# Kernel tuning notes

Hardware: AMD Instinct MI355X
Metric: run time of the kernel (lower is better)

Reference implementation:

```python
import jax, jax.numpy as jnp
import numpy as np

B, T, D_Q, D_V, ATTN, FILTERS, KSIZE = 64, 2048, 1024, 512, 128, 32, 31


def setup_inputs() -> dict:
    key = jax.random.key(0)
    ks = jax.random.split(key, 10)
    query = jax.random.normal(ks[0], (B, D_Q), dtype=jnp.float32)
    values = jax.random.normal(ks[1], (B, T, D_V), dtype=jnp.float32)
    keys = jax.random.normal(ks[2], (B, T, ATTN), dtype=jnp.float32)
    state = jax.random.uniform(ks[3], (B, T), dtype=jnp.float32)
    # learned parameters
    W_q = jax.random.normal(ks[4], (D_Q, ATTN), dtype=jnp.float32) * 0.02
    conv_kernel = jax.random.normal(ks[5], (KSIZE, 1, FILTERS), dtype=jnp.float32) * 0.1  # (W, In, Out)
    conv_bias = jnp.zeros((FILTERS,), dtype=jnp.float32)
    W_loc = jax.random.normal(ks[6], (FILTERS, ATTN), dtype=jnp.float32) * 0.1
    v_att = jax.random.normal(ks[7], (ATTN, 1), dtype=jnp.float32) * 0.1
    att_bias = jax.random.normal(ks[8], (ATTN,), dtype=jnp.float32) * 0.02
    return {"query": query, "values": values, "keys": keys, "state": state,
            "W_q": W_q, "conv_kernel": conv_kernel, "conv_bias": conv_bias,
            "W_loc": W_loc, "v_att": v_att, "att_bias": att_bias}


def reference(query, values, keys, state, W_q, conv_kernel, conv_bias, W_loc, v_att, att_bias):
    # processed_query: [B, 1, ATTN]
    pq = (query @ W_q)[:, None, :]
    # location features: Conv1D same-padding over alignments [B, T, 1] -> [B, T, FILTERS]
    loc = jax.lax.conv_general_dilated(
        state[:, :, None], conv_kernel,
        window_strides=(1,), padding='SAME',
        dimension_numbers=('NWC', 'WIO', 'NWC')) + conv_bias
    ploc = loc @ W_loc                                  # [B, T, ATTN]
    score = jnp.tanh(keys + pq + ploc + att_bias) @ v_att  # [B, T, 1]
    alignment = jax.nn.softmax(score, axis=1)           # [B, T, 1]
    attention = jnp.sum(alignment * values, axis=1)     # [B, D_V]
    alignment = jnp.squeeze(alignment, axis=2)          # [B, T]
    attention_state = alignment + state                 # cumulate=True
    return (attention, alignment, attention_state)
```

## Files before the change

### kernel.cpp

```cpp
#include <hip/hip_runtime.h>
#include <hip/hip_bf16.h>

#define B 64
#define T 2048
#define D_Q 1024
#define D_V 512
#define ATTN 128
#define FILTERS 32
#define KSIZE 31

#define PQ_OFF 0
#define CW_OFF 8192
#define PB_OFF (8192 + 3968)
#define SC_OFF (8192 + 3968 + 128)
#define ML_OFF (SC_OFF + 131072)
#define PART_OFF (ML_OFF + 4096)

#define AT_OFF 0
#define AL_OFF 32768
#define ST_OFF (32768 + 131072)

typedef float v4f __attribute__((ext_vector_type(4)));

__device__ __forceinline__ float4 nt_load4(const float4* p) {
    v4f v = __builtin_nontemporal_load((const v4f*)p);
    return make_float4(v.x, v.y, v.z, v.w);
}

__device__ __forceinline__ float tanh_fast(float x) {
    float e = __expf(2.f * x);
    return 1.f - 2.f / (e + 1.f);
}

__global__ void __launch_bounds__(256)
k1_precompute(const float* __restrict__ query,
              const float* __restrict__ Wq,
              const float* __restrict__ ck,
              const float* __restrict__ cbias,
              const float* __restrict__ Wl,
              const float* __restrict__ abias,
              float* __restrict__ ws) {
    int tid = threadIdx.x;
    if (blockIdx.x < B) {
        int b = blockIdx.x;
        int q = tid & 31;
        int s = tid >> 5;
        __shared__ __align__(16) float sq[D_Q];
        __shared__ float4 red[256];
        ((float4*)sq)[tid] = ((const float4*)(query + (size_t)b * D_Q))[tid];
        __syncthreads();

        const float4* Wq4 = (const float4*)Wq;
        float4 acc = make_float4(0.f, 0.f, 0.f, 0.f);
        int dbase = s << 7;
#pragma unroll 16
        for (int i = 0; i < 128; ++i) {
            int d = dbase + i;
            float sd = sq[d];
            float4 w = Wq4[(size_t)d * 32 + q];
            acc.x += sd * w.x; acc.y += sd * w.y;
            acc.z += sd * w.z; acc.w += sd * w.w;
        }
        red[tid] = acc;
        __syncthreads();
        if (tid < 128) {
            float4 o = red[tid + 128];
            acc = red[tid];
            acc.x += o.x; acc.y += o.y; acc.z += o.z; acc.w += o.w;
            red[tid] = acc;
        }
        __syncthreads();
        if (tid < 64) {
            float4 o = red[tid + 64];
            acc = red[tid];
            acc.x += o.x; acc.y += o.y; acc.z += o.z; acc.w += o.w;
            red[tid] = acc;
        }
        __syncthreads();
        if (tid < 32) {
            float4 o = red[tid + 32];
            acc = red[tid];
            acc.x += o.x; acc.y += o.y; acc.z += o.z; acc.w += o.w;
            ((float4*)(ws + PQ_OFF))[b * 32 + tid] = acc;
        }
    } else {
        __shared__ float swl[FILTERS * ATTN];
        for (int i = tid; i < FILTERS * ATTN; i += 256) swl[i] = Wl[i];
        __syncthreads();
        if (tid < ATTN) {
            int a = tid;
            for (int k = 0; k < KSIZE; ++k) {
                float acc = 0.f;
#pragma unroll
                for (int f = 0; f < FILTERS; ++f) acc += ck[k * FILTERS + f] * swl[f * ATTN + a];
                ws[CW_OFF + k * ATTN + a] = acc;
            }
            float pb = abias[a];
#pragma unroll
            for (int f = 0; f < FILTERS; ++f) pb += cbias[f] * swl[f * ATTN + a];
            ws[PB_OFF + a] = pb;
        }
    }
}

__global__ void __launch_bounds__(256)
k2_fused(const float* __restrict__ keys,
         const float* __restrict__ state,
         const float* __restrict__ values,
         const float* __restrict__ vatt,
         float* __restrict__ ws) {
    int bid = blockIdx.x;
    int b = bid >> 5;
    int c = bid & 31;
    int t0 = c << 6;
    int tid = threadIdx.x;
    int a4 = tid & 31;
    int h = tid >> 5;

    __shared__ __align__(16) float sstate[96];
    __shared__ __align__(16) float scw[KSIZE][ATTN];
    __shared__ float sred[64];
    __shared__ float sal[64];
    __shared__ float4 spart[128];

    if (tid < 96) {
        int idx = t0 + tid - 15;
        sstate[tid] = (idx >= 0 && idx < T) ? state[b * T + idx] : 0.f;
    }
    {
        const float4* cw4 = (const float4*)(ws + CW_OFF);
        float4* dst = (float4*)&scw[0][0];
        for (int i = tid; i < (KSIZE * ATTN) / 4; i += 256) dst[i] = cw4[i];
    }

    float4 pq4, vat4;
    {
        float4 pq = ((const float4*)(ws + PQ_OFF))[b * 32 + a4];
        float4 pb = ((const float4*)(ws + PB_OFF))[a4];
        pq4 = make_float4(pq.x + pb.x, pq.y + pb.y, pq.z + pb.z, pq.w + pb.w);
        vat4 = ((const float4*)vatt)[a4];
    }
    __syncthreads();

    {
        const float4* sv = (const float4*)sstate;
        float w[40];
        int wq0 = h << 1;
#pragma unroll
        for (int q = 0; q < 10; ++q) {
            float4 v = sv[wq0 + q];
            w[4 * q + 0] = v.x; w[4 * q + 1] = v.y;
            w[4 * q + 2] = v.z; w[4 * q + 3] = v.w;
        }

        const float4* K4 = (const float4*)keys
                           + ((size_t)b * T + t0 + h * 8) * (ATTN / 4) + a4;
        float4 kv[8];
#pragma unroll
        for (int j = 0; j < 8; ++j)
            kv[j] = nt_load4(&K4[(size_t)j * (ATTN / 4)]);

        float4 acc[8];
#pragma unroll
        for (int j = 0; j < 8; ++j) acc[j] = make_float4(0.f, 0.f, 0.f, 0.f);
#pragma unroll
        for (int k = 0; k < KSIZE; ++k) {
            float4 cwk = ((const float4*)&scw[k][0])[a4];
#pragma unroll
            for (int j = 0; j < 8; ++j) {
                float wv = w[j + k];
                acc[j].x += wv * cwk.x; acc[j].y += wv * cwk.y;
                acc[j].z += wv * cwk.z; acc[j].w += wv * cwk.w;
            }
        }
#pragma unroll
        for (int j = 0; j < 8; ++j) {
            float xx = kv[j].x + pq4.x + acc[j].x;
            float xy = kv[j].y + pq4.y + acc[j].y;
            float xz = kv[j].z + pq4.z + acc[j].z;
            float xw = kv[j].w + pq4.w + acc[j].w;
            float cc = tanh_fast(xx) * vat4.x + tanh_fast(xy) * vat4.y
                     + tanh_fast(xz) * vat4.z + tanh_fast(xw) * vat4.w;
#pragma unroll
            for (int off = 16; off >= 1; off >>= 1) cc += __shfl_xor(cc, off);
            if (a4 == 0) sred[h * 8 + j] = cc;
        }
    }
    __syncthreads();

    if (tid < 64) {
        float s = sred[tid];
        ws[SC_OFF + b * T + t0 + tid] = s;
        float m = s;
#pragma unroll
        for (int off = 32; off >= 1; off >>= 1) m = fmaxf(m, __shfl_xor(m, off));
        float e = __expf(s - m);
        sal[tid] = e;
        float l = e;
#pragma unroll
        for (int off = 32; off >= 1; off >>= 1) l += __shfl_xor(l, off);
        if (tid == 0) {
            ws[ML_OFF + (b * 32 + c) * 2 + 0] = m;
            ws[ML_OFF + (b * 32 + c) * 2 + 1] = l;
        }
    }
    __syncthreads();

    int d4 = tid & 127;
    int hc = tid >> 7;
    const float4* V = (const float4*)values + ((size_t)b * T + t0) * (D_V / 4) + d4;
    float4 acc = make_float4(0.f, 0.f, 0.f, 0.f);
#pragma unroll 8
    for (int i = 0; i < 32; ++i) {
        int tl = hc * 32 + i;
        float al = sal[tl];
        float4 v = nt_load4(&V[(size_t)tl * (D_V / 4)]);
        acc.x += al * v.x; acc.y += al * v.y;
        acc.z += al * v.z; acc.w += al * v.w;
    }
    if (hc == 1) spart[d4] = acc;
    __syncthreads();
    if (hc == 0) {
        float4 o = spart[d4];
        acc.x += o.x; acc.y += o.y; acc.z += o.z; acc.w += o.w;
        ((float4*)(ws + PART_OFF))[(size_t)(b * 32 + c) * (D_V / 4) + d4] = acc;
    }
}

__global__ void __launch_bounds__(256)
k_combine(const float* __restrict__ state,
          const float* __restrict__ ws,
          float* __restrict__ out) {
    int b = blockIdx.x >> 2;
    int r = blockIdx.x & 3;
    int tid = threadIdx.x;
    __shared__ float sw[32];
    __shared__ float sM, sinvL;

    if (tid < 32) {
        float m = ws[ML_OFF + (b * 32 + tid) * 2 + 0];
        float l = ws[ML_OFF + (b * 32 + tid) * 2 + 1];
        float M = m;
#pragma unroll
        for (int off = 16; off >= 1; off >>= 1) M = fmaxf(M, __shfl_xor(M, off));
        float wgt = __expf(m - M);
        sw[tid] = wgt;
        float L = l * wgt;
#pragma unroll
        for (int off = 16; off >= 1; off >>= 1) L += __shfl_xor(L, off);
        if (tid == 0) { sM = M; sinvL = 1.f / L; }
    }
    __syncthreads();

    float M = sM, invL = sinvL;

    if (tid < 128) {
        int d = (r << 7) + tid;
        float acc = 0.f;
#pragma unroll 8
        for (int c = 0; c < 32; ++c)
            acc += sw[c] * ws[PART_OFF + (size_t)(b * 32 + c) * D_V + d];
        out[AT_OFF + b * D_V + d] = acc * invL;
    }

#pragma unroll
    for (int k = 0; k < 2; ++k) {
        int t = (r << 9) + tid + (k << 8);
        float s = ws[SC_OFF + b * T + t];
        float al = __expf(s - M) * invL;
        out[AL_OFF + b * T + t] = al;
        out[ST_OFF + b * T + t] = al + state[b * T + t];
    }
}

extern "C" void kernel_launch(void* const* d_in, const int* in_sizes, int n_in,
                              void* d_out, int out_size, void* d_ws, size_t ws_size,
                              hipStream_t stream) {
    const float* query  = (const float*)d_in[0];
    const float* values = (const float*)d_in[1];
    const float* keys   = (const float*)d_in[2];
    const float* state  = (const float*)d_in[3];
    const float* Wq     = (const float*)d_in[4];
    const float* ck     = (const float*)d_in[5];
    const float* cbias  = (const float*)d_in[6];
    const float* Wl     = (const float*)d_in[7];
    const float* vatt   = (const float*)d_in[8];
    const float* abias  = (const float*)d_in[9];
    float* out = (float*)d_out;
    float* ws  = (float*)d_ws;

    k1_precompute<<<B + 1, 256, 0, stream>>>(query, Wq, ck, cbias, Wl, abias, ws);
    k2_fused<<<B * (T / 64), 256, 0, stream>>>(keys, state, values, vatt, ws);
    k_combine<<<B * 4, 256, 0, stream>>>(state, ws, out);
}
```

Baseline: 417.6 us.

## Fuse softmax combine into main kernel via last-block atomic counter

```diff
diff --git a/kernel.cpp b/kernel.cpp
--- a/kernel.cpp
+++ b/kernel.cpp
@@ -15,6 +15,7 @@
 #define SC_OFF (8192 + 3968 + 128)
 #define ML_OFF (SC_OFF + 131072)
 #define PART_OFF (ML_OFF + 4096)
+#define CNT_OFF (PART_OFF + 1048576)
 
 #define AT_OFF 0
 #define AL_OFF 32768
@@ -86,6 +87,7 @@
     } else {
         __shared__ float swl[FILTERS * ATTN];
         for (int i = tid; i < FILTERS * ATTN; i += 256) swl[i] = Wl[i];
+        if (tid < B) ((int*)ws)[CNT_OFF + tid] = 0;
         __syncthreads();
         if (tid < ATTN) {
             int a = tid;
@@ -108,7 +110,8 @@
          const float* __restrict__ state,
          const float* __restrict__ values,
          const float* __restrict__ vatt,
-         float* __restrict__ ws) {
+         float* __restrict__ ws,
+         float* __restrict__ out) {
     int bid = blockIdx.x;
     int b = bid >> 5;
     int c = bid & 31;
@@ -206,37 +209,41 @@
     }
     __syncthreads();
 
-    int d4 = tid & 127;
-    int hc = tid >> 7;
-    const float4* V = (const float4*)values + ((size_t)b * T + t0) * (D_V / 4) + d4;
-    float4 acc = make_float4(0.f, 0.f, 0.f, 0.f);
+    {
+        int d4 = tid & 127;
+        int hc = tid >> 7;
+        const float4* V = (const float4*)values + ((size_t)b * T + t0) * (D_V / 4) + d4;
+        float4 acc = make_float4(0.f, 0.f, 0.f, 0.f);
 #pragma unroll 8
-    for (int i = 0; i < 32; ++i) {
-        int tl = hc * 32 + i;
-        float al = sal[tl];
-        float4 v = nt_load4(&V[(size_t)tl * (D_V / 4)]);
-        acc.x += al * v.x; acc.y += al * v.y;
-        acc.z += al * v.z; acc.w += al * v.w;
-    }
-    if (hc == 1) spart[d4] = acc;
-    __syncthreads();
-    if (hc == 0) {
-        float4 o = spart[d4];
-        acc.x += o.x; acc.y += o.y; acc.z += o.z; acc.w += o.w;
-        ((float4*)(ws + PART_OFF))[(size_t)(b * 32 + c) * (D_V / 4) + d4] = acc;
-    }
-}
-
-__global__ void __launch_bounds__(256)
-k_combine(const float* __restrict__ state,
-          const float* __restrict__ ws,
-          float* __restrict__ out) {
-    int b = blockIdx.x >> 2;
-    int r = blockIdx.x & 3;
-    int tid = threadIdx.x;
+        for (int i = 0; i < 32; ++i) {
+            int tl = hc * 32 + i;
+            float al = sal[tl];
+            float4 v = nt_load4(&V[(size_t)tl * (D_V / 4)]);
+            acc.x += al * v.x; acc.y += al * v.y;
+            acc.z += al * v.z; acc.w += al * v.w;
+        }
+        if (hc == 1) spart[d4] = acc;
+        __syncthreads();
+        if (hc == 0) {
+            float4 o = spart[d4];
+            acc.x += o.x; acc.y += o.y; acc.z += o.z; acc.w += o.w;
+            ((float4*)(ws + PART_OFF))[(size_t)(b * 32 + c) * (D_V / 4) + d4] = acc;
+        }
+    }
+
+    __shared__ int slast;
+    __syncthreads();
+    if (tid == 0) {
+        __threadfence();
+        int old = atomicAdd(&((int*)ws)[CNT_OFF + b], 1);
+        slast = (old == 31);
+    }
+    __syncthreads();
+    if (!slast) return;
+    __threadfence();
+
     __shared__ float sw[32];
     __shared__ float sM, sinvL;
-
     if (tid < 32) {
         float m = ws[ML_OFF + (b * 32 + tid) * 2 + 0];
         float l = ws[ML_OFF + (b * 32 + tid) * 2 + 1];
@@ -254,18 +261,19 @@
 
     float M = sM, invL = sinvL;
 
-    if (tid < 128) {
-        int d = (r << 7) + tid;
+#pragma unroll
+    for (int r = 0; r < 2; ++r) {
+        int d = tid + (r << 8);
         float acc = 0.f;
 #pragma unroll 8
-        for (int c = 0; c < 32; ++c)
-            acc += sw[c] * ws[PART_OFF + (size_t)(b * 32 + c) * D_V + d];
+        for (int cc = 0; cc < 32; ++cc)
+            acc += sw[cc] * ws[PART_OFF + (size_t)(b * 32 + cc) * D_V + d];
         out[AT_OFF + b * D_V + d] = acc * invL;
     }
 
 #pragma unroll
-    for (int k = 0; k < 2; ++k) {
-        int t = (r << 9) + tid + (k << 8);
+    for (int k = 0; k < 8; ++k) {
+        int t = tid + (k << 8);
         float s = ws[SC_OFF + b * T + t];
         float al = __expf(s - M) * invL;
         out[AL_OFF + b * T + t] = al;
@@ -290,6 +298,5 @@
     float* ws  = (float*)d_ws;
 
     k1_precompute<<<B + 1, 256, 0, stream>>>(query, Wq, ck, cbias, Wl, abias, ws);
-    k2_fused<<<B * (T / 64), 256, 0, stream>>>(keys, state, values, vatt, ws);
-    k_combine<<<B * 4, 256, 0, stream>>>(state, ws, out);
-}
+    k2_fused<<<B * (T / 64), 256, 0, stream>>>(keys, state, values, vatt, ws, out);
+}
```

Result: slower. 578.9 us (+38.6%).
